# Kernel tuning notes

Hardware: AMD Instinct MI355X
Metric: run time of the kernel (lower is better)

## Reference

```python
import jax, jax.numpy as jnp
import numpy as np

N_HEADS = 16
EMBED = 1024
HEAD_SIZE = 64
BLOCK = 2048
BATCH = 4


def setup_inputs() -> dict:
    key = jax.random.key(0)
    ks = jax.random.split(key, 6)
    s = 1.0 / np.sqrt(EMBED)
    X = jax.random.normal(ks[0], (BATCH, BLOCK, EMBED), dtype=jnp.float32)
    Wq = jax.random.normal(ks[1], (N_HEADS, EMBED, HEAD_SIZE), dtype=jnp.float32) * s
    Wk = jax.random.normal(ks[2], (N_HEADS, EMBED, HEAD_SIZE), dtype=jnp.float32) * s
    Wv = jax.random.normal(ks[3], (N_HEADS, EMBED, HEAD_SIZE), dtype=jnp.float32) * s
    Wo = jax.random.normal(ks[4], (EMBED, EMBED), dtype=jnp.float32) * s
    bo = jnp.zeros((EMBED,), dtype=jnp.float32)
    return {"X": X, "Wq": Wq, "Wk": Wk, "Wv": Wv, "Wo": Wo, "bo": bo}


def reference(X, Wq, Wk, Wv, Wo, bo):
    # X: [B, S, E]; Wq/Wk/Wv: [H, E, Dh]
    q = jnp.einsum("bse,hed->bhsd", X, Wq)
    k = jnp.einsum("bse,hed->bhsd", X, Wk)
    v = jnp.einsum("bse,hed->bhsd", X, Wv)
    scale = 1.0 / np.sqrt(HEAD_SIZE)
    scores = jnp.einsum("bhsd,bhtd->bhst", q, k) * scale  # [B,H,S,S]
    S = X.shape[1]
    causal = jnp.tril(jnp.ones((S, S), dtype=bool))
    scores = jnp.where(causal, scores, -jnp.inf)
    wei = jax.nn.softmax(scores, axis=-1)
    # dropout p=0.2 treated as identity (eval mode) for deterministic reference
    out = jnp.einsum("bhst,bhtd->bhsd", wei, v)  # [B,H,S,Dh]
    out = out.transpose(0, 2, 1, 3).reshape(X.shape[0], S, N_HEADS * HEAD_SIZE)
    return out @ Wo.T + bo
```

## Files before the change

kernel.cpp:

```cpp
#include <hip/hip_runtime.h>
#include <stdint.h>


typedef __bf16 bf16_t;
typedef __bf16 bf16x4 __attribute__((ext_vector_type(4)));
typedef __bf16 bf16x8 __attribute__((ext_vector_type(8)));
typedef float  f32x4  __attribute__((ext_vector_type(4)));
typedef float  f32x16 __attribute__((ext_vector_type(16)));
typedef unsigned int u32;

union V8 { bf16x8 v8; bf16x4 h[2]; u32 w[4]; };

__device__ __forceinline__ void gload_lds16(const void* g, void* l) {
  __builtin_amdgcn_global_load_lds((const __attribute__((address_space(1))) void*)g,
                                   (__attribute__((address_space(3))) void*)l, 16, 0, 0);
}


__global__ __launch_bounds__(256) void mha_prep_all(const float* __restrict__ X,
                                                    const float* __restrict__ Wq,
                                                    const float* __restrict__ Wk,
                                                    const float* __restrict__ Wv,
                                                    const float* __restrict__ Wo,
                                                    bf16_t* __restrict__ Xb,
                                                    bf16_t* __restrict__ Wob,
                                                    bf16_t* __restrict__ Wt) {
  const int bx = blockIdx.x;
  if (bx < 4608) {
    const float* src = (bx < 4096) ? X : Wo;
    bf16_t* dst = (bx < 4096) ? Xb : Wob;
    size_t base = (size_t)((bx < 4096) ? bx : bx - 4096) * 256 + threadIdx.x;
    size_t i = base * 8;
    const float4* p = (const float4*)(src + i);
    float4 a = p[0], b = p[1];
    bf16x8 o;
    o[0] = (__bf16)a.x; o[1] = (__bf16)a.y; o[2] = (__bf16)a.z; o[3] = (__bf16)a.w;
    o[4] = (__bf16)b.x; o[5] = (__bf16)b.y; o[6] = (__bf16)b.z; o[7] = (__bf16)b.w;
    *(bf16x8*)(dst + i) = o;
  } else {
    __shared__ float tile[64][65];
    const int pid = bx - 4608;
    const int e0 = (pid & 15) * 64;
    const int mh = pid >> 4;
    const int mat = mh >> 4, h = mh & 15;
    const float* W = (mat == 0) ? Wq : (mat == 1) ? Wk : Wv;
    const float sc = (mat == 0) ? 0.18033688011112042f : 1.0f;
    #pragma unroll
    for (int i = 0; i < 16; i++) {
      int idx = threadIdx.x + i * 256;
      int er = idx >> 6, d = idx & 63;
      tile[er][d] = W[(size_t)(h * 1024 + e0 + er) * 64 + d];
    }
    __syncthreads();
    #pragma unroll
    for (int i = 0; i < 16; i++) {
      int idx = threadIdx.x + i * 256;
      int dr = idx >> 6, ec = idx & 63;
      Wt[(size_t)(mat * 1024 + h * 64 + dr) * 1024 + e0 + ec] = (bf16_t)(tile[ec][dr] * sc);
    }
  }
}


__global__ __launch_bounds__(512, 2) void gemm192(const bf16_t* __restrict__ A,
                                                  const bf16_t* __restrict__ Bt,
                                                  bf16_t* __restrict__ C,
                                                  int M, int N, int K) {
  __shared__ __align__(16) char lds[131072];
  const int tid = threadIdx.x;
  const int l = tid & 63, w = tid >> 6;
  const int g = l >> 4, lg = l & 15;
  const int wr = w >> 2, wc = w & 3;
  const int bid = blockIdx.x;
  const int nbn = N / 192;
  const int gsw = (bid & 7) * (gridDim.x >> 3) + (bid >> 3);
  const long brow = (long)(gsw / nbn) * 256;
  const long bcol = (long)(gsw % nbn) * 192;

  f32x4 acc[8][3];
  #pragma unroll
  for (int im = 0; im < 8; im++)
    #pragma unroll
    for (int n = 0; n < 3; n++) acc[im][n] = (f32x4){0.f, 0.f, 0.f, 0.f};

  auto stage = [&](const bf16_t* base, long trow, int k0, int region, bool pad) {
    #pragma unroll
    for (int j = 0; j < 2; j++) {
      int p = (tid + j * 512) * 16;
      int row = p >> 6, slot = (p >> 4) & 3;
      int src = slot ^ ((row >> 1) & 3);
      int r2 = (pad && row >= 192) ? row - 192 : row;
      gload_lds16(base + (trow + r2) * (long)K + k0 + src * 8,
                  lds + region + p);
    }
  };

  stage(A,  brow, 0,  0,              false);
  stage(Bt, bcol, 0,  65536,          true);
  stage(A,  brow, 32, 16384,          false);
  stage(Bt, bcol, 32, 65536 + 16384,  true);
  stage(A,  brow, 64, 32768,          false);
  stage(Bt, bcol, 64, 65536 + 32768,  true);
  asm volatile("s_waitcnt vmcnt(4)" ::: "memory");
  __builtin_amdgcn_s_barrier();
  __builtin_amdgcn_sched_barrier(0);

  const int sw = (lg >> 1) & 3;
  const int nIter = K >> 7;
  for (int t = 0; t < nIter; t++) {
    const bool more = (t + 1 < nIter);
    const int kb = t * 128;
    #pragma unroll
    for (int ph = 0; ph < 8; ph++) {
      const int slot = ph >> 2;
      const int kh = (ph >> 1) & 1, mq = ph & 1;
      bf16x8 af[4], bfv[3];
      {
        const char* pA = lds + slot * 32768 + kh * 16384;
        const char* pB = pA + 65536;
        #pragma unroll
        for (int m = 0; m < 4; m++) {
          int wrow = wr * 128 + mq * 64 + m * 16 + lg;
          af[m] = *(const bf16x8*)(pA + wrow * 64 + ((g ^ sw) << 4));
        }
        #pragma unroll
        for (int n = 0; n < 3; n++) {
          int wrow = wc * 48 + n * 16 + lg;
          bfv[n] = *(const bf16x8*)(pB + wrow * 64 + ((g ^ sw) << 4));
        }
      }
      if (ph == 0)      stage(A,  brow, kb + 96,  32768 + 16384, false);
      else if (ph == 1) stage(Bt, bcol, kb + 96,  65536 + 32768 + 16384, true);
      else if (more) {
        if (ph == 2)      stage(A,  brow, kb + 128, 0, false);
        else if (ph == 3) stage(Bt, bcol, kb + 128, 65536, true);
        else if (ph == 4) stage(A,  brow, kb + 160, 16384, false);
        else if (ph == 5) stage(Bt, bcol, kb + 160, 65536 + 16384, true);
        else if (ph == 6) stage(A,  brow, kb + 192, 32768, false);
        else              stage(Bt, bcol, kb + 192, 65536 + 32768, true);
      }
      __builtin_amdgcn_s_barrier();
      asm volatile("s_waitcnt lgkmcnt(0)" ::: "memory");
      __builtin_amdgcn_sched_barrier(0);
      __builtin_amdgcn_s_setprio(1);
      #pragma unroll
      for (int m = 0; m < 4; m++)
        #pragma unroll
        for (int n = 0; n < 3; n++)
          acc[mq * 4 + m][n] =
              __builtin_amdgcn_mfma_f32_16x16x32_bf16(af[m], bfv[n], acc[mq * 4 + m][n], 0, 0, 0);
      __builtin_amdgcn_s_setprio(0);
      __builtin_amdgcn_sched_barrier(0);
      if (ph == 3) {
        if (more) asm volatile("s_waitcnt vmcnt(4)" ::: "memory");
        else      asm volatile("s_waitcnt vmcnt(0)" ::: "memory");
      } else if (ph == 7 && more) {
        asm volatile("s_waitcnt vmcnt(4)" ::: "memory");
      }
      __builtin_amdgcn_s_barrier();
      __builtin_amdgcn_sched_barrier(0);
    }
  }

  #pragma unroll
  for (int im = 0; im < 8; im++)
    #pragma unroll
    for (int n = 0; n < 3; n++) {
      long row0 = brow + wr * 128 + im * 16 + g * 4;
      long col  = bcol + wc * 48 + n * 16 + lg;
      #pragma unroll
      for (int r = 0; r < 4; r++)
        C[(row0 + r) * N + col] = (bf16_t)acc[im][n][r];
    }
}


template <int MODE>
__global__ __launch_bounds__(256) void gemm_bt(const bf16_t* __restrict__ A,
                                               const bf16_t* __restrict__ Bt,
                                               void* __restrict__ Cout,
                                               const float* __restrict__ bias,
                                               int M, int N, int K) {
  __shared__ bf16_t lA[128 * 32];
  __shared__ bf16_t lB[128 * 32];
  const int tid = threadIdx.x;
  const int l = tid & 63, w = tid >> 6;
  const int g = l >> 4, lg = l & 15;
  const int wr = w >> 1, wc = w & 1;
  const long brow = (long)blockIdx.y * 128;
  const long bcol = (long)blockIdx.x * 128;

  f32x4 acc[4][4];
  #pragma unroll
  for (int m = 0; m < 4; m++)
    #pragma unroll
    for (int n = 0; n < 4; n++) acc[m][n] = (f32x4){0.f, 0.f, 0.f, 0.f};

  const bf16_t* Ab = A + brow * K;
  const bf16_t* Bb = Bt + bcol * K;
  const int c0 = tid, c1 = tid + 256;
  const int r0 = c0 >> 2, o0 = (c0 & 3) * 8;
  const int r1 = c1 >> 2, o1 = (c1 & 3) * 8;

  for (int k0 = 0; k0 < K; k0 += 32) {
    __syncthreads();
    gload_lds16(Ab + (long)r0 * K + k0 + o0, lA + c0 * 8);
    gload_lds16(Ab + (long)r1 * K + k0 + o1, lA + c1 * 8);
    gload_lds16(Bb + (long)r0 * K + k0 + o0, lB + c0 * 8);
    gload_lds16(Bb + (long)r1 * K + k0 + o1, lB + c1 * 8);
    __syncthreads();
    bf16x8 af[4], bfr[4];
    #pragma unroll
    for (int m = 0; m < 4; m++)
      af[m] = *(const bf16x8*)(lA + (wr * 64 + m * 16 + lg) * 32 + g * 8);
    #pragma unroll
    for (int n = 0; n < 4; n++)
      bfr[n] = *(const bf16x8*)(lB + (wc * 64 + n * 16 + lg) * 32 + g * 8);
    #pragma unroll
    for (int m = 0; m < 4; m++)
      #pragma unroll
      for (int n = 0; n < 4; n++)
        acc[m][n] = __builtin_amdgcn_mfma_f32_16x16x32_bf16(af[m], bfr[n], acc[m][n], 0, 0, 0);
  }

  #pragma unroll
  for (int m = 0; m < 4; m++) {
    #pragma unroll
    for (int n = 0; n < 4; n++) {
      long row0 = brow + wr * 64 + m * 16 + g * 4;
      long col  = bcol + wc * 64 + n * 16 + lg;
      if (MODE == 0) {
        bf16_t* Cb = (bf16_t*)Cout;
        #pragma unroll
        for (int r = 0; r < 4; r++) Cb[(row0 + r) * N + col] = (bf16_t)acc[m][n][r];
      } else {
        float* Cf = (float*)Cout;
        float bv = bias[col];
        #pragma unroll
        for (int r = 0; r < 4; r++) Cf[(row0 + r) * N + col] = acc[m][n][r] + bv;
      }
    }
  }
}


__global__ __launch_bounds__(256, 4) void mha_attn3(const bf16_t* __restrict__ QKV,
                                                    bf16_t* __restrict__ AO) {
  __shared__ __align__(16) char smem[32768];
  const int tid = threadIdx.x;
  const int l = tid & 63, w = tid >> 6;
  const int q31 = l & 31;
  const int hi = l >> 5;
  const int hb = (l >> 4) & 1;
  const int lg = l & 15;

  const int bid = blockIdx.x;
  const int xcd = bid & 7, ii = bid >> 3;
  const int bh = xcd * 8 + (ii & 7);
  const int stripe = 15 - (ii >> 3);
  const int b = bh >> 4, h = bh & 15;

  const int qw = stripe * 128 + w * 32;
  const bf16_t* Qp = QKV + (size_t)b * 2048 * 3072 + h * 64;
  const bf16_t* Kp = Qp + 1024;
  const bf16_t* Vp = Qp + 2048;

  bf16x8 qf[4];
  {
    const bf16_t* qrow = Qp + (size_t)(qw + q31) * 3072 + hi * 8;
    #pragma unroll
    for (int ks = 0; ks < 4; ks++) qf[ks] = *(const bf16x8*)(qrow + ks * 16);
  }

  f32x16 o0, o1, z16;
  #pragma unroll
  for (int r = 0; r < 16; r++) { o0[r] = 0.f; o1[r] = 0.f; z16[r] = 0.f; }
  float lsum = 0.f;

  const int tmaxw = 2 * stripe + 1 + (w >> 1);
  const int T = 2 * stripe + 2;
  const u32 ldsbase = (u32)(uintptr_t)(__attribute__((address_space(3))) char*)smem;

  const int krow = tid >> 3, kcb = (tid & 7) * 16;
  const int kscb = kcb ^ ((krow & 7) << 4);
  const int st0 = tid >> 5, qq0 = tid & 31;
  const int st1 = (tid + 256) >> 5, qq1 = qq0;
  const bf16_t* kp0 = Kp + (size_t)krow * 3072 + (kscb >> 1);
  const bf16_t* kp1 = kp0 + (size_t)32 * 3072;
  const bf16_t* vp0 = Vp + (size_t)((st0 >> 2) * 16 + (qq0 >> 1)) * 3072 + (st0 & 3) * 16 + (qq0 & 1) * 8;
  const bf16_t* vp1 = Vp + (size_t)((st1 >> 2) * 16 + (qq1 >> 1)) * 3072 + (st1 & 3) * 16 + (qq1 & 1) * 8;
  const size_t KVSTEP = (size_t)64 * 3072;

  auto stage = [&](int bi) {
    char* kb = smem + bi * 8192;
    char* vb = smem + 16384 + bi * 8192;
    gload_lds16(kp0, kb + tid * 16);
    gload_lds16(vp0, vb + tid * 16);
    gload_lds16(kp1, kb + (tid + 256) * 16);
    gload_lds16(vp1, vb + (tid + 256) * 16);
    kp0 += KVSTEP; kp1 += KVSTEP; vp0 += KVSTEP; vp1 += KVSTEP;
  };

  stage(0);
  for (int t = 0; t < T; t++) {
    const int cur = t & 1;
    if (t + 1 < T) {
      stage(cur ^ 1);
      __builtin_amdgcn_sched_barrier(0);
      asm volatile("s_waitcnt vmcnt(4)" ::: "memory");
    } else {
      __builtin_amdgcn_sched_barrier(0);
      asm volatile("s_waitcnt vmcnt(0)" ::: "memory");
    }
    __builtin_amdgcn_sched_barrier(0);
    __builtin_amdgcn_s_barrier();
    __builtin_amdgcn_sched_barrier(0);

    const bool active = (t < tmaxw);
    u32 paw[4][4];
    if (active) {
      f32x16 p0, p1;
      {
        const char* kb = smem + cur * 8192;
        const int rb0 = q31 * 128;
        const int swz = (l & 7) << 4;
        __builtin_amdgcn_s_setprio(1);
        {
          int colb = (hi << 4) ^ swz;
          bf16x8 kf0 = *(const bf16x8*)(kb + rb0 + colb);
          bf16x8 kf1 = *(const bf16x8*)(kb + 4096 + rb0 + colb);
          p0 = __builtin_amdgcn_mfma_f32_32x32x16_bf16(kf0, qf[0], z16, 0, 0, 0);
          p1 = __builtin_amdgcn_mfma_f32_32x32x16_bf16(kf1, qf[0], z16, 0, 0, 0);
        }
        #pragma unroll
        for (int ks = 1; ks < 4; ks++) {
          int colb = ((ks << 5) | (hi << 4)) ^ swz;
          bf16x8 kf0 = *(const bf16x8*)(kb + rb0 + colb);
          bf16x8 kf1 = *(const bf16x8*)(kb + 4096 + rb0 + colb);
          p0 = __builtin_amdgcn_mfma_f32_32x32x16_bf16(kf0, qf[ks], p0, 0, 0, 0);
          p1 = __builtin_amdgcn_mfma_f32_32x32x16_bf16(kf1, qf[ks], p1, 0, 0, 0);
        }
        __builtin_amdgcn_s_setprio(0);
      }
      if (t == tmaxw - 1) {
        int q = qw + q31;
        int kvb = t * 64 + 4 * hi;
        #pragma unroll
        for (int r = 0; r < 16; r++) {
          int kv0 = kvb + (r & 3) + 8 * (r >> 2);
          if (kv0 > q) p0[r] = -1e30f;
          if (kv0 + 32 > q) p1[r] = -1e30f;
        }
      }
      #pragma unroll
      for (int r = 0; r < 16; r++) p0[r] = exp2f(p0[r]);
      #pragma unroll
      for (int r = 0; r < 16; r++) p1[r] = exp2f(p1[r]);
      float s8[8];
      #pragma unroll
      for (int r = 0; r < 8; r++)
        s8[r] = (p0[r] + p0[r + 8]) + (p1[r] + p1[r + 8]);
      float rs = ((s8[0] + s8[1]) + (s8[2] + s8[3])) + ((s8[4] + s8[5]) + (s8[6] + s8[7]));
      rs += __shfl_xor(rs, 32);
      lsum += rs;
      #pragma unroll
      for (int gblk = 0; gblk < 4; gblk++) {
        int base = (gblk & 1) * 8;
        float e0 = (gblk < 2) ? p0[base + 0] : p1[base + 0];
        float e1 = (gblk < 2) ? p0[base + 1] : p1[base + 1];
        float e2 = (gblk < 2) ? p0[base + 2] : p1[base + 2];
        float e3 = (gblk < 2) ? p0[base + 3] : p1[base + 3];
        float e4 = (gblk < 2) ? p0[base + 4] : p1[base + 4];
        float e5 = (gblk < 2) ? p0[base + 5] : p1[base + 5];
        float e6 = (gblk < 2) ? p0[base + 6] : p1[base + 6];
        float e7 = (gblk < 2) ? p0[base + 7] : p1[base + 7];
        u32 u0, u1, v0, v1;
        asm("v_cvt_pk_bf16_f32 %0, %1, %2" : "=v"(u0) : "v"(e0), "v"(e1));
        asm("v_cvt_pk_bf16_f32 %0, %1, %2" : "=v"(u1) : "v"(e2), "v"(e3));
        asm("v_cvt_pk_bf16_f32 %0, %1, %2" : "=v"(v0) : "v"(e4), "v"(e5));
        asm("v_cvt_pk_bf16_f32 %0, %1, %2" : "=v"(v1) : "v"(e6), "v"(e7));
        asm("v_permlane32_swap_b32 %0, %1" : "+v"(u0), "+v"(v0));
        asm("v_permlane32_swap_b32 %0, %1" : "+v"(u1), "+v"(v1));
        paw[gblk][0] = u0; paw[gblk][1] = u1; paw[gblk][2] = v0; paw[gblk][3] = v1;
      }
      V8 vf[2][4];
      u32 vb = ldsbase + 16384u + (u32)cur * 8192u;
      #pragma unroll
      for (int mb = 0; mb < 2; mb++)
        #pragma unroll
        for (int ks = 0; ks < 4; ks++) {
          u32 base = vb + (u32)(((ks * 4 + 2 * mb + hb) << 9) + hi * 256 + lg * 8);
          bf16x4 t0, t1;
          asm volatile("ds_read_b64_tr_b16 %0, %1" : "=v"(t0) : "v"(base));
          asm volatile("ds_read_b64_tr_b16 %0, %1 offset:128" : "=v"(t1) : "v"(base));
          vf[mb][ks].h[0] = t0; vf[mb][ks].h[1] = t1;
        }
      asm volatile("s_waitcnt lgkmcnt(0)" ::: "memory");
      __builtin_amdgcn_sched_barrier(0);
      __builtin_amdgcn_s_setprio(1);
      #pragma unroll
      for (int ks = 0; ks < 4; ks++) {
        V8 pa; pa.w[0] = paw[ks][0]; pa.w[1] = paw[ks][1]; pa.w[2] = paw[ks][2]; pa.w[3] = paw[ks][3];
        o0 = __builtin_amdgcn_mfma_f32_32x32x16_bf16(vf[0][ks].v8, pa.v8, o0, 0, 0, 0);
        o1 = __builtin_amdgcn_mfma_f32_32x32x16_bf16(vf[1][ks].v8, pa.v8, o1, 0, 0, 0);
      }
      __builtin_amdgcn_s_setprio(0);
    }
    __builtin_amdgcn_sched_barrier(0);
    __builtin_amdgcn_s_barrier();
    __builtin_amdgcn_sched_barrier(0);
  }

  float linv = 1.f / lsum;
  __syncthreads();
  bf16_t* ow = (bf16_t*)smem + w * 2048;
  #pragma unroll
  for (int mb = 0; mb < 2; mb++)
    #pragma unroll
    for (int r = 0; r < 16; r += 2) {
      int d = mb * 32 + (r & 3) + 8 * (r >> 2) + 4 * hi;
      float a0 = (mb ? o1[r] : o0[r]) * linv;
      float a1 = (mb ? o1[r + 1] : o0[r + 1]) * linv;
      u32 pk;
      asm("v_cvt_pk_bf16_f32 %0, %1, %2" : "=v"(pk) : "v"(a0), "v"(a1));
      int byteoff = q31 * 128 + ((d * 2) ^ ((q31 & 7) << 4));
      *(u32*)((char*)ow + byteoff) = pk;
    }
  __syncthreads();
  const size_t aorow0 = (size_t)b * 2048 + qw;
  #pragma unroll
  for (int it = 0; it < 4; it++) {
    int idx = it * 64 + l;
    int q = idx >> 3, cc = idx & 7;
    bf16x8 v8 = *(const bf16x8*)((const char*)ow + q * 128 + ((cc * 16) ^ ((q & 7) << 4)));
    *(bf16x8*)(AO + (aorow0 + q) * 1024 + h * 64 + cc * 8) = v8;
  }
}


extern "C" void kernel_launch(void* const* d_in, const int* in_sizes, int n_in,
                              void* d_out, int out_size, void* d_ws, size_t ws_size,
                              hipStream_t stream) {
  (void)in_sizes; (void)n_in; (void)out_size; (void)ws_size;
  const float* X  = (const float*)d_in[0];
  const float* Wq = (const float*)d_in[1];
  const float* Wk = (const float*)d_in[2];
  const float* Wv = (const float*)d_in[3];
  const float* Wo = (const float*)d_in[4];
  const float* bo = (const float*)d_in[5];
  float* out = (float*)d_out;

  char* ws = (char*)d_ws;
  bf16_t* Xb  = (bf16_t*)ws;
  bf16_t* AO  = Xb;
  bf16_t* Wt  = (bf16_t*)(ws + (16u << 20));
  bf16_t* Wob = (bf16_t*)(ws + (22u << 20));
  bf16_t* QKV = (bf16_t*)(ws + (24u << 20));

  mha_prep_all<<<dim3(5376), dim3(256), 0, stream>>>(X, Wq, Wk, Wv, Wo, Xb, Wob, Wt);
  gemm192<<<dim3(512), dim3(512), 0, stream>>>(Xb, Wt, QKV, 8192, 3072, 1024);
  mha_attn3<<<dim3(1024), dim3(256), 0, stream>>>(QKV, AO);
  gemm_bt<1><<<dim3(1024 / 128, 8192 / 128), dim3(256), 0, stream>>>(
      AO, Wob, (void*)out, bo, 8192, 1024, 1024);
}
```

Baseline: 170.6 us.

## Triple-buffer K/V tiles in attention and drop the trailing barrier per tile

```diff
diff --git a/kernel.cpp b/kernel.cpp
--- a/kernel.cpp
+++ b/kernel.cpp
@@ -151,11 +151,9 @@
               __builtin_amdgcn_mfma_f32_16x16x32_bf16(af[m], bfv[n], acc[mq * 4 + m][n], 0, 0, 0);
       __builtin_amdgcn_s_setprio(0);
       __builtin_amdgcn_sched_barrier(0);
-      if (ph == 3) {
+      if (ph & 1) {
         if (more) asm volatile("s_waitcnt vmcnt(4)" ::: "memory");
-        else      asm volatile("s_waitcnt vmcnt(0)" ::: "memory");
-      } else if (ph == 7 && more) {
-        asm volatile("s_waitcnt vmcnt(4)" ::: "memory");
+        else if (ph == 1) asm volatile("s_waitcnt vmcnt(0)" ::: "memory");
       }
       __builtin_amdgcn_s_barrier();
       __builtin_amdgcn_sched_barrier(0);
@@ -244,9 +242,9 @@
 }
 
 
-__global__ __launch_bounds__(256, 4) void mha_attn3(const bf16_t* __restrict__ QKV,
+__global__ __launch_bounds__(256, 3) void mha_attn4(const bf16_t* __restrict__ QKV,
                                                     bf16_t* __restrict__ AO) {
-  __shared__ __align__(16) char smem[32768];
+  __shared__ __align__(16) char smem[49152];
   const int tid = threadIdx.x;
   const int l = tid & 63, w = tid >> 6;
   const int q31 = l & 31;
@@ -281,19 +279,27 @@
   const int T = 2 * stripe + 2;
   const u32 ldsbase = (u32)(uintptr_t)(__attribute__((address_space(3))) char*)smem;
 
+  u32 vb0[2][4];
+  #pragma unroll
+  for (int mb = 0; mb < 2; mb++)
+    #pragma unroll
+    for (int ks = 0; ks < 4; ks++)
+      vb0[mb][ks] = ldsbase + 24576u +
+                    (u32)(((ks * 4 + 2 * mb + hb) << 9) + hi * 256 + lg * 8);
+
   const int krow = tid >> 3, kcb = (tid & 7) * 16;
   const int kscb = kcb ^ ((krow & 7) << 4);
   const int st0 = tid >> 5, qq0 = tid & 31;
-  const int st1 = (tid + 256) >> 5, qq1 = qq0;
+  const int st1 = (tid + 256) >> 5;
   const bf16_t* kp0 = Kp + (size_t)krow * 3072 + (kscb >> 1);
   const bf16_t* kp1 = kp0 + (size_t)32 * 3072;
   const bf16_t* vp0 = Vp + (size_t)((st0 >> 2) * 16 + (qq0 >> 1)) * 3072 + (st0 & 3) * 16 + (qq0 & 1) * 8;
-  const bf16_t* vp1 = Vp + (size_t)((st1 >> 2) * 16 + (qq1 >> 1)) * 3072 + (st1 & 3) * 16 + (qq1 & 1) * 8;
+  const bf16_t* vp1 = Vp + (size_t)((st1 >> 2) * 16 + (qq0 >> 1)) * 3072 + (st1 & 3) * 16 + (qq0 & 1) * 8;
   const size_t KVSTEP = (size_t)64 * 3072;
 
   auto stage = [&](int bi) {
     char* kb = smem + bi * 8192;
-    char* vb = smem + 16384 + bi * 8192;
+    char* vb = smem + 24576 + bi * 8192;
     gload_lds16(kp0, kb + tid * 16);
     gload_lds16(vp0, vb + tid * 16);
     gload_lds16(kp1, kb + (tid + 256) * 16);
@@ -302,10 +308,11 @@
   };
 
   stage(0);
+  int cur3 = 0;
   for (int t = 0; t < T; t++) {
-    const int cur = t & 1;
+    int nxt3 = cur3 + 1; if (nxt3 == 3) nxt3 = 0;
     if (t + 1 < T) {
-      stage(cur ^ 1);
+      stage(nxt3);
       __builtin_amdgcn_sched_barrier(0);
       asm volatile("s_waitcnt vmcnt(4)" ::: "memory");
     } else {
@@ -321,7 +328,7 @@
     if (active) {
       f32x16 p0, p1;
       {
-        const char* kb = smem + cur * 8192;
+        const char* kb = smem + cur3 * 8192;
         const int rb0 = q31 * 128;
         const int swz = (l & 7) << 4;
         __builtin_amdgcn_s_setprio(1);
@@ -384,12 +391,12 @@
         paw[gblk][0] = u0; paw[gblk][1] = u1; paw[gblk][2] = v0; paw[gblk][3] = v1;
       }
       V8 vf[2][4];
-      u32 vb = ldsbase + 16384u + (u32)cur * 8192u;
+      const u32 boff = (u32)cur3 * 8192u;
       #pragma unroll
       for (int mb = 0; mb < 2; mb++)
         #pragma unroll
         for (int ks = 0; ks < 4; ks++) {
-          u32 base = vb + (u32)(((ks * 4 + 2 * mb + hb) << 9) + hi * 256 + lg * 8);
+          u32 base = vb0[mb][ks] + boff;
           bf16x4 t0, t1;
           asm volatile("ds_read_b64_tr_b16 %0, %1" : "=v"(t0) : "v"(base));
           asm volatile("ds_read_b64_tr_b16 %0, %1 offset:128" : "=v"(t1) : "v"(base));
@@ -406,9 +413,7 @@
       }
       __builtin_amdgcn_s_setprio(0);
     }
-    __builtin_amdgcn_sched_barrier(0);
-    __builtin_amdgcn_s_barrier();
-    __builtin_amdgcn_sched_barrier(0);
+    cur3 = nxt3;
   }
 
   float linv = 1.f / lsum;
@@ -459,7 +464,7 @@
 
   mha_prep_all<<<dim3(5376), dim3(256), 0, stream>>>(X, Wq, Wk, Wv, Wo, Xb, Wob, Wt);
   gemm192<<<dim3(512), dim3(512), 0, stream>>>(Xb, Wt, QKV, 8192, 3072, 1024);
-  mha_attn3<<<dim3(1024), dim3(256), 0, stream>>>(QKV, AO);
+  mha_attn4<<<dim3(1024), dim3(256), 0, stream>>>(QKV, AO);
   gemm_bt<1><<<dim3(1024 / 128, 8192 / 128), dim3(256), 0, stream>>>(
       AO, Wob, (void*)out, bo, 8192, 1024, 1024);
 }
```

New measurement: 167.7 us. About the same (-1.7%).
